# Performance work log

Measured on AMD Instinct MI355X. Metric: run time of the kernel, lower is better.

The kernel has to match this reference:

```python
import jax, jax.numpy as jnp
import numpy as np

B, T, C = 4, 2048, 1024
H = 16
D = C // H  # head_size = 64


def setup_inputs() -> dict:
    key = jax.random.key(0)
    ks = jax.random.split(key, 6)
    s = 0.02
    x = jax.random.normal(ks[0], (B, T, C), dtype=jnp.float32)
    # per-head projections (bias=False), stacked over heads: [H, C, D]
    Wq = jax.random.normal(ks[1], (H, C, D), dtype=jnp.float32) * s
    Wk = jax.random.normal(ks[2], (H, C, D), dtype=jnp.float32) * s
    Wv = jax.random.normal(ks[3], (H, C, D), dtype=jnp.float32) * s
    # output projection Linear(H*D, C)
    Wo = jax.random.normal(ks[4], (H * D, C), dtype=jnp.float32) * s
    bo = jax.random.normal(ks[5], (C,), dtype=jnp.float32) * s
    return {"x": x, "Wq": Wq, "Wk": Wk, "Wv": Wv, "Wo": Wo, "bo": bo}


def reference(x, Wq, Wk, Wv, Wo, bo):
    # q,k,v: [B, H, T, D]
    q = jnp.einsum('btc,hcd->bhtd', x, Wq)
    k = jnp.einsum('btc,hcd->bhtd', x, Wk)
    v = jnp.einsum('btc,hcd->bhtd', x, Wv)
    scale = 1.0 / jnp.sqrt(jnp.asarray(D, dtype=x.dtype))
    scores = jnp.einsum('bhtd,bhsd->bhts', q, k) * scale  # [B,H,T,T]
    causal = jnp.tril(jnp.ones((T, T), dtype=bool))
    scores = jnp.where(causal, scores, jnp.asarray(-jnp.inf, dtype=scores.dtype))
    wei = jax.nn.softmax(scores, axis=-1)
    out = jnp.einsum('bhts,bhsd->bhtd', wei, v)  # [B,H,T,D]
    # concat heads along last dim (head order = module list order)
    out = jnp.transpose(out, (0, 2, 1, 3)).reshape(B, T, H * D)
    return out @ Wo + bo
```

## Files before the change

kernel.cpp:

```cpp
#include <hip/hip_runtime.h>
#include <math.h>

typedef __attribute__((ext_vector_type(8))) short short8;
typedef __attribute__((ext_vector_type(4))) short short4v;
typedef __attribute__((ext_vector_type(4))) float floatx4;

#define AS1 __attribute__((address_space(1)))
#define AS3 __attribute__((address_space(3)))

__device__ inline void gload_lds16(const short* g, short* l) {
    __builtin_amdgcn_global_load_lds((const AS1 unsigned int*)g,
                                     (AS3 unsigned int*)l, 16, 0, 0);
}

__device__ inline short f2bf(float f) {
    unsigned u = __builtin_bit_cast(unsigned, f);
    u += 0x7fffu + ((u >> 16) & 1u);
    return (short)(u >> 16);
}

__global__ __launch_bounds__(256) void conv_x(
    const float* __restrict__ x, short* __restrict__ xb)
{
    int i = (blockIdx.x * 256 + threadIdx.x) * 4;
    float4 v = *(const float4*)&x[i];
    short4v o = { f2bf(v.x), f2bf(v.y), f2bf(v.z), f2bf(v.w) };
    *(short4v*)&xb[i] = o;
}

__global__ __launch_bounds__(256) void transpose_w(
    const float* __restrict__ Wq, const float* __restrict__ Wk,
    const float* __restrict__ Wv, const float* __restrict__ Wo,
    short* __restrict__ Wall, short* __restrict__ WoT)
{
    __shared__ short T[64 * 72];
    const int kt = blockIdx.x, y = blockIdx.y;
    const int tid = threadIdx.x;
    const int lr = tid >> 2, lc = (tid & 3) * 16;
    #pragma unroll 1
    for (int m = 0; m < 4; ++m) {
        const float* src;
        float s = 1.f;
        if (m < 3) {
            const float* W = (m == 0) ? Wq : (m == 1) ? Wk : Wv;
            src = W + ((size_t)y << 16) + (size_t)(kt * 64 + lr) * 64 + lc;
            if (m == 0) s = 0.125f;
        } else {
            src = Wo + (size_t)(kt * 64 + lr) * 1024 + y * 64 + lc;
        }
        short8 t0, t1;
        #pragma unroll
        for (int c = 0; c < 2; ++c) {
            float4 a = *(const float4*)(src + c * 8);
            float4 b = *(const float4*)(src + c * 8 + 4);
            t0[c*4+0] = f2bf(a.x*s); t0[c*4+1] = f2bf(a.y*s);
            t0[c*4+2] = f2bf(a.z*s); t0[c*4+3] = f2bf(a.w*s);
            float4 a2 = *(const float4*)(src + 8 + c * 8);
            (void)a2; (void)b;
        }
        {
            float4 v0 = *(const float4*)(src + 0);
            float4 v1 = *(const float4*)(src + 4);
            float4 v2 = *(const float4*)(src + 8);
            float4 v3 = *(const float4*)(src + 12);
            t0[0]=f2bf(v0.x*s); t0[1]=f2bf(v0.y*s); t0[2]=f2bf(v0.z*s); t0[3]=f2bf(v0.w*s);
            t0[4]=f2bf(v1.x*s); t0[5]=f2bf(v1.y*s); t0[6]=f2bf(v1.z*s); t0[7]=f2bf(v1.w*s);
            t1[0]=f2bf(v2.x*s); t1[1]=f2bf(v2.y*s); t1[2]=f2bf(v2.z*s); t1[3]=f2bf(v2.w*s);
            t1[4]=f2bf(v3.x*s); t1[5]=f2bf(v3.y*s); t1[6]=f2bf(v3.z*s); t1[7]=f2bf(v3.w*s);
        }
        *(short8*)&T[lr * 72 + lc]     = t0;
        *(short8*)&T[lr * 72 + lc + 8] = t1;
        __syncthreads();
        short8 o0, o1;
        #pragma unroll
        for (int j = 0; j < 8; ++j) o0[j] = T[(lc + j) * 72 + lr];
        #pragma unroll
        for (int j = 0; j < 8; ++j) o1[j] = T[(lc + 8 + j) * 72 + lr];
        short* dst = (m < 3)
            ? Wall + (size_t)(m * 1024 + y * 64 + lr) * 1024 + kt * 64
            : WoT  + (size_t)(y * 64 + lr) * 1024 + kt * 64;
        *(short8*)&dst[lc]     = o0;
        *(short8*)&dst[lc + 8] = o1;
        __syncthreads();
    }
}

__global__ __launch_bounds__(256) void transpose_v(
    const short* __restrict__ Vp, short* __restrict__ Vt_g)
{
    __shared__ short T[64 * 72];
    const int t0 = blockIdx.x * 64;
    const int h = blockIdx.y, b = blockIdx.z;
    const int tid = threadIdx.x;
    const int r = tid >> 3, c = (tid & 7) * 8;
    #pragma unroll
    for (int p = 0; p < 2; ++p) {
        int t = r + 32 * p;
        *(short8*)&T[t * 72 + c] =
            *(const short8*)&Vp[(size_t)(b * 2048 + t0 + t) * 1024 + h * 64 + c];
    }
    __syncthreads();
    const int d = tid >> 2, tc = (tid & 3) * 16;
    size_t obase = ((size_t)(b * 16 + h)) * 64 * 2048 + (size_t)d * 2048 + t0 + tc;
    short8 o0, o1;
    #pragma unroll
    for (int j = 0; j < 8; ++j) o0[j] = T[(tc + j) * 72 + d];
    #pragma unroll
    for (int j = 0; j < 8; ++j) o1[j] = T[(tc + 8 + j) * 72 + d];
    *(short8*)&Vt_g[obase] = o0;
    *(short8*)&Vt_g[obase + 8] = o1;
}

__global__ __launch_bounds__(256) void gemm_bt(
    const short* __restrict__ A, const short* __restrict__ BT,
    short* __restrict__ C, short* __restrict__ Cv, float* __restrict__ Cf,
    const float* __restrict__ bias, int M, int N, int K, int split)
{
    __shared__ short As[128 * 32];
    __shared__ short Bs[128 * 32];
    const int tid  = threadIdx.x;
    const int wid  = tid >> 6, lane = tid & 63;
    const int quad = lane >> 4, l15 = lane & 15;
    const int m0 = blockIdx.x * 128, n0 = blockIdx.y * 128;
    const int wr = (wid >> 1) * 64, wc = (wid & 1) * 64;

    floatx4 acc[4][4] = {};

    const int srow = wid * 32 + (lane >> 2);
    const int scol = (lane & 3) * 8;

    for (int k0 = 0; k0 < K; k0 += 32) {
        #pragma unroll
        for (int t = 0; t < 2; ++t) {
            gload_lds16(A  + (size_t)(m0 + srow + t * 16) * K + k0 + scol,
                        &As[(wid * 32 + t * 16) * 32]);
            gload_lds16(BT + (size_t)(n0 + srow + t * 16) * K + k0 + scol,
                        &Bs[(wid * 32 + t * 16) * 32]);
        }
        __syncthreads();
        short8 bfr[4];
        #pragma unroll
        for (int j = 0; j < 4; ++j)
            bfr[j] = *(const short8*)&Bs[(wc + j * 16 + l15) * 32 + quad * 8];
        #pragma unroll
        for (int i = 0; i < 4; ++i) {
            short8 afr = *(const short8*)&As[(wr + i * 16 + l15) * 32 + quad * 8];
            #pragma unroll
            for (int j = 0; j < 4; ++j)
                acc[i][j] = __builtin_amdgcn_mfma_f32_16x16x32_bf16(
                    afr, bfr[j], acc[i][j], 0, 0, 0);
        }
        __syncthreads();
    }

    #pragma unroll
    for (int i = 0; i < 4; ++i) {
        int row = m0 + wr + i * 16 + quad * 4;
        #pragma unroll
        for (int j = 0; j < 4; ++j) {
            int col = n0 + wc + j * 16 + l15;
            if (Cf) {
                float bv = bias ? bias[col] : 0.f;
                #pragma unroll
                for (int r = 0; r < 4; ++r)
                    Cf[(size_t)(row + r) * N + col] = acc[i][j][r] + bv;
            } else if (split) {
                int plane = col >> 10, c1 = col & 1023;
                short* dst = (plane == 2) ? Cv
                           : C + (size_t)plane * 8192 * 1024;
                #pragma unroll
                for (int r = 0; r < 4; ++r)
                    dst[(size_t)(row + r) * 1024 + c1] = f2bf(acc[i][j][r]);
            } else {
                #pragma unroll
                for (int r = 0; r < 4; ++r)
                    C[(size_t)(row + r) * 1024 + col] = f2bf(acc[i][j][r]);
            }
        }
    }
}

__global__ __launch_bounds__(256) void attn_fwd(
    const short* __restrict__ Q, const short* __restrict__ Kg,
    const short* __restrict__ Vt_g, short* __restrict__ O)
{
    __shared__ short Ks[2][64 * 72];
    __shared__ short Vs[2][64 * 72];
    __shared__ short Pb[4 * 32 * 72];
    const int tid  = threadIdx.x;
    const int wid  = tid >> 6, lane = tid & 63;
    const int quad = lane >> 4, l15 = lane & 15;
    const int pi = blockIdx.x, h = blockIdx.y, b = blockIdx.z;
    const size_t base  = ((size_t)b * 2048) * 1024 + h * 64;
    const size_t vbase = ((size_t)(b * 16 + h)) * 64 * 2048;
    const int sr = tid >> 3, sc = (tid & 7) * 8;
    short* Pw = &Pb[wid * 32 * 72];

    for (int ph = 0; ph < 2; ++ph) {
        const int qt = ph ? pi : 15 - pi;
        short8 qf[2][2];
        #pragma unroll
        for (int mt = 0; mt < 2; ++mt)
            #pragma unroll
            for (int ks = 0; ks < 2; ++ks)
                qf[mt][ks] = *(const short8*)&Q[base +
                    (size_t)(qt * 128 + wid * 32 + mt * 16 + l15) * 1024 + ks * 32 + quad * 8];

        float lsum[2][4] = {};
        floatx4 oacc[2][4] = {};
        const int dst = 2 * qt + (wid >> 1);
        const int nst = 2 * qt + 2;

        short8 kv[2], vv[2];
        #pragma unroll
        for (int p = 0; p < 2; ++p) {
            int row = sr + 32 * p;
            kv[p] = *(const short8*)&Kg[base + (size_t)row * 1024 + sc];
            vv[p] = *(const short8*)&Vt_g[vbase + (size_t)row * 2048 + sc];
        }
        #pragma unroll
        for (int p = 0; p < 2; ++p) {
            int row = sr + 32 * p;
            *(short8*)&Ks[0][row * 72 + sc] = kv[p];
            *(short8*)&Vs[0][row * 72 + sc] = vv[p];
        }
        #pragma unroll
        for (int p = 0; p < 2; ++p) {
            int row = sr + 32 * p;
            kv[p] = *(const short8*)&Kg[base + (size_t)(64 + row) * 1024 + sc];
            vv[p] = *(const short8*)&Vt_g[vbase + (size_t)row * 2048 + 64 + sc];
        }
        __syncthreads();

        for (int st = 0; st < nst; ++st) {
            const short* K0 = Ks[st & 1];
            const short* V0 = Vs[st & 1];
            if (st + 1 < nst) {
                short* K1 = Ks[(st + 1) & 1];
                short* V1 = Vs[(st + 1) & 1];
                #pragma unroll
                for (int p = 0; p < 2; ++p) {
                    int row = sr + 32 * p;
                    *(short8*)&K1[row * 72 + sc] = kv[p];
                    *(short8*)&V1[row * 72 + sc] = vv[p];
                }
            }
            if (st + 2 < nst) {
                #pragma unroll
                for (int p = 0; p < 2; ++p) {
                    int row = sr + 32 * p;
                    kv[p] = *(const short8*)&Kg[base + (size_t)((st + 2) * 64 + row) * 1024 + sc];
                    vv[p] = *(const short8*)&Vt_g[vbase + (size_t)row * 2048 + (st + 2) * 64 + sc];
                }
            }

            if (st <= dst) {
                floatx4 sf[2][4];
                #pragma unroll
                for (int nt = 0; nt < 4; ++nt) {
                    floatx4 z0 = {}, z1 = {};
                    #pragma unroll
                    for (int ks = 0; ks < 2; ++ks) {
                        short8 bfr = *(const short8*)&K0[(nt * 16 + l15) * 72 + ks * 32 + quad * 8];
                        z0 = __builtin_amdgcn_mfma_f32_16x16x32_bf16(qf[0][ks], bfr, z0, 0, 0, 0);
                        z1 = __builtin_amdgcn_mfma_f32_16x16x32_bf16(qf[1][ks], bfr, z1, 0, 0, 0);
                    }
                    sf[0][nt] = z0; sf[1][nt] = z1;
                }

                if (st == dst) {
                    #pragma unroll
                    for (int mt = 0; mt < 2; ++mt)
                        #pragma unroll
                        for (int nt = 0; nt < 4; ++nt)
                            #pragma unroll
                            for (int r = 0; r < 4; ++r) {
                                int qa = qt * 128 + wid * 32 + mt * 16 + quad * 4 + r;
                                int sa = st * 64 + nt * 16 + l15;
                                if (sa > qa) sf[mt][nt][r] = -INFINITY;
                            }
                }

                #pragma unroll
                for (int mt = 0; mt < 2; ++mt)
                    #pragma unroll
                    for (int nt = 0; nt < 4; ++nt)
                        #pragma unroll
                        for (int r = 0; r < 4; ++r) {
                            float p = __expf(sf[mt][nt][r]);
                            lsum[mt][r] += p;
                            unsigned u = __builtin_bit_cast(unsigned, p) + 0x8000u;
                            Pw[(mt * 16 + quad * 4 + r) * 72 + ((nt ^ quad) * 16) + l15] =
                                (short)(u >> 16);
                        }

                #pragma unroll
                for (int ks = 0; ks < 2; ++ks) {
                    int blk = (ks * 2 + (quad >> 1)) ^ (l15 >> 2);
                    short8 af0 = *(const short8*)&Pw[(l15) * 72 + blk * 16 + (quad & 1) * 8];
                    short8 af1 = *(const short8*)&Pw[(16 + l15) * 72 + blk * 16 + (quad & 1) * 8];
                    #pragma unroll
                    for (int nt = 0; nt < 4; ++nt) {
                        short8 bfr = *(const short8*)&V0[(nt * 16 + l15) * 72 + ks * 32 + quad * 8];
                        oacc[0][nt] = __builtin_amdgcn_mfma_f32_16x16x32_bf16(af0, bfr, oacc[0][nt], 0, 0, 0);
                        oacc[1][nt] = __builtin_amdgcn_mfma_f32_16x16x32_bf16(af1, bfr, oacc[1][nt], 0, 0, 0);
                    }
                }
            }
            __syncthreads();
        }

        #pragma unroll
        for (int mt = 0; mt < 2; ++mt)
            #pragma unroll
            for (int r = 0; r < 4; ++r) {
                float s = lsum[mt][r];
                #pragma unroll
                for (int off = 1; off < 16; off <<= 1)
                    s += __shfl_xor(s, off, 64);
                lsum[mt][r] = s;
            }

        #pragma unroll
        for (int mt = 0; mt < 2; ++mt)
            #pragma unroll
            for (int nt = 0; nt < 4; ++nt)
                #pragma unroll
                for (int r = 0; r < 4; ++r) {
                    float v = oacc[mt][nt][r] / lsum[mt][r];
                    int qa = qt * 128 + wid * 32 + mt * 16 + quad * 4 + r;
                    O[base + (size_t)qa * 1024 + nt * 16 + l15] = f2bf(v);
                }
    }
}

extern "C" void kernel_launch(void* const* d_in, const int* in_sizes, int n_in,
                              void* d_out, int out_size, void* d_ws, size_t ws_size,
                              hipStream_t stream) {
    const float* x  = (const float*)d_in[0];
    const float* Wq = (const float*)d_in[1];
    const float* Wk = (const float*)d_in[2];
    const float* Wv = (const float*)d_in[3];
    const float* Wo = (const float*)d_in[4];
    const float* bo = (const float*)d_in[5];
    float* out = (float*)d_out;

    char* ws = (char*)d_ws;
    const size_t MB = 1024 * 1024;
    short* xb   = (short*)(ws + 0 * MB);
    short* Vt_g = (short*)(ws + 0 * MB);
    short* Vr   = (short*)(ws + 16 * MB);
    short* Ao   = (short*)(ws + 16 * MB);
    short* Wall = (short*)(ws + 32 * MB);
    short* WoT  = (short*)(ws + 38 * MB);
    short* Qp   = (short*)d_out;
    short* Kp   = Qp + 8 * 1024 * 1024;

    conv_x<<<8192, 256, 0, stream>>>(x, xb);
    transpose_w<<<dim3(16, 16), 256, 0, stream>>>(Wq, Wk, Wv, Wo, Wall, WoT);

    gemm_bt<<<dim3(64, 24), 256, 0, stream>>>(xb, Wall, Qp, Vr, nullptr, nullptr,
                                              8192, 3072, 1024, 1);
    transpose_v<<<dim3(32, 16, 4), 256, 0, stream>>>(Vr, Vt_g);

    attn_fwd<<<dim3(8, 16, 4), 256, 0, stream>>>(Qp, Kp, Vt_g, Ao);

    gemm_bt<<<dim3(64, 8), 256, 0, stream>>>(Ao, WoT, nullptr, nullptr, out, bo,
                                             8192, 1024, 1024, 0);
}
```

Baseline: 288.6 us.

## Fold log2e into Q scale, use exp2, compute row sums via MFMA with ones

Folds log2(e) into the Q weight scale so the softmax exponent can use exp2f directly instead of __expf. The per-element running row-sum accumulation and the final cross-lane shuffle reduction are replaced by an MFMA that multiplies the bf16 P tile by a vector of ones. This also makes the denominator consistent with the rounded P values. K/V prefetch addressing is switched to incrementing pointers, and dead loads are removed from the weight transpose. The MFMA row sum adds matrix work per step but frees VALU adds and shuffles.

```diff
diff --git a/kernel.cpp b/kernel.cpp
--- a/kernel.cpp
+++ b/kernel.cpp
@@ -44,20 +44,11 @@
         if (m < 3) {
             const float* W = (m == 0) ? Wq : (m == 1) ? Wk : Wv;
             src = W + ((size_t)y << 16) + (size_t)(kt * 64 + lr) * 64 + lc;
-            if (m == 0) s = 0.125f;
+            if (m == 0) s = 0.125f * 1.44269504088896f;
         } else {
             src = Wo + (size_t)(kt * 64 + lr) * 1024 + y * 64 + lc;
         }
         short8 t0, t1;
-        #pragma unroll
-        for (int c = 0; c < 2; ++c) {
-            float4 a = *(const float4*)(src + c * 8);
-            float4 b = *(const float4*)(src + c * 8 + 4);
-            t0[c*4+0] = f2bf(a.x*s); t0[c*4+1] = f2bf(a.y*s);
-            t0[c*4+2] = f2bf(a.z*s); t0[c*4+3] = f2bf(a.w*s);
-            float4 a2 = *(const float4*)(src + 8 + c * 8);
-            (void)a2; (void)b;
-        }
         {
             float4 v0 = *(const float4*)(src + 0);
             float4 v1 = *(const float4*)(src + 4);
@@ -196,6 +187,10 @@
     const int sr = tid >> 3, sc = (tid & 7) * 8;
     short* Pw = &Pb[wid * 32 * 72];
 
+    const short one_bf = (short)0x3F80;
+    const short8 bones = { one_bf, one_bf, one_bf, one_bf,
+                           one_bf, one_bf, one_bf, one_bf };
+
     for (int ph = 0; ph < 2; ++ph) {
         const int qt = ph ? pi : 15 - pi;
         short8 qf[2][2];
@@ -206,18 +201,21 @@
                 qf[mt][ks] = *(const short8*)&Q[base +
                     (size_t)(qt * 128 + wid * 32 + mt * 16 + l15) * 1024 + ks * 32 + quad * 8];
 
-        float lsum[2][4] = {};
         floatx4 oacc[2][4] = {};
+        floatx4 lacc[2] = {};
         const int dst = 2 * qt + (wid >> 1);
         const int nst = 2 * qt + 2;
 
+        const short* kcur = Kg + base + (size_t)sr * 1024 + sc;
+        const short* vcur = Vt_g + vbase + (size_t)sr * 2048 + sc;
+
         short8 kv[2], vv[2];
         #pragma unroll
         for (int p = 0; p < 2; ++p) {
-            int row = sr + 32 * p;
-            kv[p] = *(const short8*)&Kg[base + (size_t)row * 1024 + sc];
-            vv[p] = *(const short8*)&Vt_g[vbase + (size_t)row * 2048 + sc];
-        }
+            kv[p] = *(const short8*)(kcur + (size_t)p * 32 * 1024);
+            vv[p] = *(const short8*)(vcur + (size_t)p * 32 * 2048);
+        }
+        kcur += 64 * 1024; vcur += 64;
         #pragma unroll
         for (int p = 0; p < 2; ++p) {
             int row = sr + 32 * p;
@@ -226,10 +224,10 @@
         }
         #pragma unroll
         for (int p = 0; p < 2; ++p) {
-            int row = sr + 32 * p;
-            kv[p] = *(const short8*)&Kg[base + (size_t)(64 + row) * 1024 + sc];
-            vv[p] = *(const short8*)&Vt_g[vbase + (size_t)row * 2048 + 64 + sc];
-        }
+            kv[p] = *(const short8*)(kcur + (size_t)p * 32 * 1024);
+            vv[p] = *(const short8*)(vcur + (size_t)p * 32 * 2048);
+        }
+        kcur += 64 * 1024; vcur += 64;
         __syncthreads();
 
         for (int st = 0; st < nst; ++st) {
@@ -248,10 +246,10 @@
             if (st + 2 < nst) {
                 #pragma unroll
                 for (int p = 0; p < 2; ++p) {
-                    int row = sr + 32 * p;
-                    kv[p] = *(const short8*)&Kg[base + (size_t)((st + 2) * 64 + row) * 1024 + sc];
-                    vv[p] = *(const short8*)&Vt_g[vbase + (size_t)row * 2048 + (st + 2) * 64 + sc];
-                }
+                    kv[p] = *(const short8*)(kcur + (size_t)p * 32 * 1024);
+                    vv[p] = *(const short8*)(vcur + (size_t)p * 32 * 2048);
+                }
+                kcur += 64 * 1024; vcur += 64;
             }
 
             if (st <= dst) {
@@ -287,8 +285,7 @@
                     for (int nt = 0; nt < 4; ++nt)
                         #pragma unroll
                         for (int r = 0; r < 4; ++r) {
-                            float p = __expf(sf[mt][nt][r]);
-                            lsum[mt][r] += p;
+                            float p = exp2f(sf[mt][nt][r]);
                             unsigned u = __builtin_bit_cast(unsigned, p) + 0x8000u;
                             Pw[(mt * 16 + quad * 4 + r) * 72 + ((nt ^ quad) * 16) + l15] =
                                 (short)(u >> 16);
@@ -299,6 +296,8 @@
                     int blk = (ks * 2 + (quad >> 1)) ^ (l15 >> 2);
                     short8 af0 = *(const short8*)&Pw[(l15) * 72 + blk * 16 + (quad & 1) * 8];
                     short8 af1 = *(const short8*)&Pw[(16 + l15) * 72 + blk * 16 + (quad & 1) * 8];
+                    lacc[0] = __builtin_amdgcn_mfma_f32_16x16x32_bf16(af0, bones, lacc[0], 0, 0, 0);
+                    lacc[1] = __builtin_amdgcn_mfma_f32_16x16x32_bf16(af1, bones, lacc[1], 0, 0, 0);
                     #pragma unroll
                     for (int nt = 0; nt < 4; ++nt) {
                         short8 bfr = *(const short8*)&V0[(nt * 16 + l15) * 72 + ks * 32 + quad * 8];
@@ -313,21 +312,10 @@
         #pragma unroll
         for (int mt = 0; mt < 2; ++mt)
             #pragma unroll
-            for (int r = 0; r < 4; ++r) {
-                float s = lsum[mt][r];
-                #pragma unroll
-                for (int off = 1; off < 16; off <<= 1)
-                    s += __shfl_xor(s, off, 64);
-                lsum[mt][r] = s;
-            }
-
-        #pragma unroll
-        for (int mt = 0; mt < 2; ++mt)
-            #pragma unroll
             for (int nt = 0; nt < 4; ++nt)
                 #pragma unroll
                 for (int r = 0; r < 4; ++r) {
-                    float v = oacc[mt][nt][r] / lsum[mt][r];
+                    float v = oacc[mt][nt][r] / lacc[mt][r];
                     int qa = qt * 128 + wid * 32 + mt * 16 + quad * 4 + r;
                     O[base + (size_t)qa * 1024 + nt * 16 + l15] = f2bf(v);
                 }
```

Result: slower. 299.1 us (+3.7%).
